# Performance work log

Measured on AMD Instinct MI355X. Metric: run time of the kernel, lower is better.

The kernel has to match this reference:

```python
import jax, jax.numpy as jnp
import numpy as np
import math

B, D, H, N, L = 32, 64, 8, 4096, 12
DK = D // H  # 8
APT = 10

def conv1x1_relu(x, w, b):
    # x: [B, C, N, L]; w: [O, C]; b: [O]  (1x1 conv == channel matmul)
    return jax.nn.relu(jnp.einsum('oc,bcnl->bonl', w, x) + b[None, :, None, None])

def setup_inputs() -> dict:
    key = jax.random.key(0)
    ks = jax.random.split(key, 12)
    s = 1.0 / math.sqrt(D)
    return {
        'x': jax.random.normal(ks[0], (B, D, N, L), jnp.float32),
        'wq': jax.random.normal(ks[1], (D, D), jnp.float32) * s,
        'bq': jnp.zeros((D,), jnp.float32),
        'wv': jax.random.normal(ks[2], (D, D), jnp.float32) * s,
        'bv': jnp.zeros((D,), jnp.float32),
        'wc': jax.random.normal(ks[3], (D, D), jnp.float32) * s,
        'bc': jnp.zeros((D,), jnp.float32),
        'memory': jax.random.normal(ks[4], (H, L, N, DK), jnp.float32) * 0.02,
        'weight': jnp.ones((D, N, L), jnp.float32),
        'bias': jnp.zeros((D, N, L), jnp.float32),
        'nv1': jax.random.normal(ks[5], (N, APT), jnp.float32),
        'nv2': jax.random.normal(ks[6], (APT, N), jnp.float32),
    }

def reference(x, wq, bq, wv, bv, wc, bc, memory, weight, bias, nv1, nv2):
    scale = 1.0 / math.sqrt(DK)
    q = conv1x1_relu(x, wq, bq)               # [B, D, N, L]
    v = conv1x1_relu(x, wv, bv)               # [B, D, N, L]
    # [B, D, N, L] -> [B, H, dk, N, L] -> [B, H, L, N, dk]
    v5 = jnp.transpose(v.reshape(B, H, DK, N, L), (0, 1, 4, 3, 2))
    q5 = jnp.transpose(q.reshape(B, H, DK, N, L), (0, 1, 4, 3, 2))
    key_sm = jax.nn.softmax(memory * scale, axis=-1)       # [H, L, N, dk]
    q_sm = jax.nn.softmax(q5 * scale, axis=-1)             # [B, H, L, N, dk]
    Aapt = jax.nn.softmax(jax.nn.relu(nv1 @ nv2), axis=-1) # [N, N]
    kv = jnp.einsum('hlnx,bhlny->bhlxy', key_sm, v5)       # [B,H,L,dk,dk]
    attn_qkv = jnp.einsum('bhlnx,bhlxy->bhlny', q_sm, kv)  # [B,H,L,N,dk]
    # 'nm,bhlnc->bhlnc' sums Aapt over m -> row-sum scaling of value
    row = jnp.sum(Aapt, axis=1)                            # [N]
    attn_dyn = row[None, None, None, :, None] * v5
    y = attn_qkv + attn_dyn                                # [B,H,L,N,dk]
    y = jnp.transpose(y, (0, 1, 4, 3, 2)).reshape(B, D, N, L)
    y = conv1x1_relu(y, wc, bc)
    out = y * weight[None] + bias[None] + y
    return out
```

## Files before the change

kernel.cpp:

```cpp
#include <hip/hip_runtime.h>
#include <math.h>

#define BB 32
#define DD 64
#define HH 8
#define NNN 4096
#define LL 12
#define PP (NNN * LL)

#define NTILES_A 24
#define CHUNK_A (64 * NTILES_A)
#define NCHUNK_A (PP / CHUNK_A)

#define NTILES_B 12
#define CHUNK_B (64 * NTILES_B)
#define NCHUNK_B (PP / CHUNK_B)

#define VSTRIDE 68
#define SCALE 0.35355339059327373f

__global__ void prep(const float* __restrict__ wq, const float* __restrict__ wv,
                     const float* __restrict__ wc, float* __restrict__ wt)
{
    const int i = blockIdx.x * 256 + threadIdx.x;
    const int o = i >> 6, c = i & 63;
    wt[c * 64 + o]        = wq[i];
    wt[4096 + c * 64 + o] = wv[i];
    wt[8192 + c * 64 + o] = wc[i];
}

__global__ void prep_ksm(const float* __restrict__ mem, float* __restrict__ ksm)
{
    const int g = blockIdx.x * 256 + threadIdx.x;
    const int p = g >> 3, h = g & 7;
    const int n = p / 12, l = p - n * 12;
    const float4* mp = (const float4*)(mem + (((size_t)(h * 12 + l) * NNN + n) << 3));
    float4 a0 = mp[0], a1 = mp[1];
    float v0 = a0.x * SCALE, v1 = a0.y * SCALE, v2 = a0.z * SCALE, v3 = a0.w * SCALE;
    float v4 = a1.x * SCALE, v5 = a1.y * SCALE, v6 = a1.z * SCALE, v7 = a1.w * SCALE;
    float m = fmaxf(fmaxf(fmaxf(v0, v1), fmaxf(v2, v3)),
                    fmaxf(fmaxf(v4, v5), fmaxf(v6, v7)));
    float e0 = __expf(v0 - m), e1 = __expf(v1 - m), e2 = __expf(v2 - m), e3 = __expf(v3 - m);
    float e4 = __expf(v4 - m), e5 = __expf(v5 - m), e6 = __expf(v6 - m), e7 = __expf(v7 - m);
    float inv = 1.0f / (e0 + e1 + e2 + e3 + e4 + e5 + e6 + e7);
    float4* op = (float4*)(ksm + ((size_t)g << 3));
    op[0] = make_float4(e0 * inv, e1 * inv, e2 * inv, e3 * inv);
    op[1] = make_float4(e4 * inv, e5 * inv, e6 * inv, e7 * inv);
}

__global__ __launch_bounds__(512, 8)
void pass_a(const float* __restrict__ x, const float* __restrict__ wvt,
            const float* __restrict__ bv, const float* __restrict__ mem,
            const float* __restrict__ ksm,
            float* __restrict__ kv)
{
    __shared__ float v_tile[64 * VSTRIDE];
    __shared__ float ks_tile[64 * VSTRIDE];

    const int t = threadIdx.x;
    const int b = blockIdx.y;
    const int chunk0 = blockIdx.x * CHUNK_A;

    const int p1 = t & 63;
    const int og = t >> 6;
    const int o0 = og << 3;
    const int o0u = __builtin_amdgcn_readfirstlane(o0);
    const float* __restrict__ wvu = wvt + o0u;

    float bvl[8];
#pragma unroll
    for (int j = 0; j < 8; j++) bvl[j] = bv[o0 + j];

    const int h2 = (t >> 3) & 7;
    const int x2 = t & 7;
    const int l0 = t >> 6;
    const int l1 = 8 + (t >> 6);
    const bool has2 = (t < 256);

    float acc[2][8];
#pragma unroll
    for (int q = 0; q < 2; q++)
#pragma unroll
        for (int y = 0; y < 8; y++) acc[q][y] = 0.f;

    const float* xb = x + (size_t)(b * 64) * PP;

    for (int tile = 0; tile < NTILES_A; tile++) {
        const int pbase = chunk0 + tile * 64;

        if (ksm) {
            const int pos = t >> 3, h = t & 7;
            const float4* kg = (const float4*)(ksm + (((size_t)(pbase + pos)) << 6) + (h << 3));
            float4 a0 = kg[0], a1 = kg[1];
            float4* kp = (float4*)(ks_tile + pos * VSTRIDE + (h << 3));
            kp[0] = a0; kp[1] = a1;
        } else {
            int pos = t >> 3, h = t & 7;
            int pg = pbase + pos;
            int n = pg / 12;
            int l = pg - n * 12;
            const float4* mp = (const float4*)(mem + (((size_t)(h * 12 + l) * NNN + n) << 3));
            float4 a0 = mp[0], a1 = mp[1];
            float v0 = a0.x * SCALE, v1 = a0.y * SCALE, v2 = a0.z * SCALE, v3 = a0.w * SCALE;
            float v4 = a1.x * SCALE, v5 = a1.y * SCALE, v6 = a1.z * SCALE, v7 = a1.w * SCALE;
            float m = fmaxf(fmaxf(fmaxf(v0, v1), fmaxf(v2, v3)),
                            fmaxf(fmaxf(v4, v5), fmaxf(v6, v7)));
            float e0 = __expf(v0 - m), e1 = __expf(v1 - m), e2 = __expf(v2 - m), e3 = __expf(v3 - m);
            float e4 = __expf(v4 - m), e5 = __expf(v5 - m), e6 = __expf(v6 - m), e7 = __expf(v7 - m);
            float inv = 1.0f / (e0 + e1 + e2 + e3 + e4 + e5 + e6 + e7);
            float4* kp = (float4*)(ks_tile + pos * VSTRIDE + (h << 3));
            kp[0] = make_float4(e0 * inv, e1 * inv, e2 * inv, e3 * inv);
            kp[1] = make_float4(e4 * inv, e5 * inv, e6 * inv, e7 * inv);
        }

        float va[8];
#pragma unroll
        for (int j = 0; j < 8; j++) va[j] = 0.f;
        const float* xp = xb + pbase + p1;
        for (int c = 0; c < 64; c += 4) {
            float xs0 = xp[(size_t)c * PP];
            float xs1 = xp[(size_t)(c + 1) * PP];
            float xs2 = xp[(size_t)(c + 2) * PP];
            float xs3 = xp[(size_t)(c + 3) * PP];
            const float* w0 = wvu + c * 64;
#pragma unroll
            for (int j = 0; j < 8; j++) {
                va[j] += w0[j] * xs0;
                va[j] += w0[64 + j] * xs1;
                va[j] += w0[128 + j] * xs2;
                va[j] += w0[192 + j] * xs3;
            }
        }
        float4* vt4 = (float4*)(v_tile + p1 * VSTRIDE + o0);
        {
            float4 w;
            w.x = fmaxf(va[0] + bvl[0], 0.f);
            w.y = fmaxf(va[1] + bvl[1], 0.f);
            w.z = fmaxf(va[2] + bvl[2], 0.f);
            w.w = fmaxf(va[3] + bvl[3], 0.f);
            vt4[0] = w;
            w.x = fmaxf(va[4] + bvl[4], 0.f);
            w.y = fmaxf(va[5] + bvl[5], 0.f);
            w.z = fmaxf(va[6] + bvl[6], 0.f);
            w.w = fmaxf(va[7] + bvl[7], 0.f);
            vt4[1] = w;
        }
        __syncthreads();

        const int r = pbase % 12;
        {
            int s = l0 - r;
            if (s < 0) s += 12;
            for (int p = s; p < 64; p += 12) {
                float ksv = ks_tile[p * VSTRIDE + (h2 << 3) + x2];
                const float4* vp = (const float4*)(v_tile + p * VSTRIDE + (h2 << 3));
                float4 u0 = vp[0], u1 = vp[1];
                acc[0][0] += ksv * u0.x; acc[0][1] += ksv * u0.y;
                acc[0][2] += ksv * u0.z; acc[0][3] += ksv * u0.w;
                acc[0][4] += ksv * u1.x; acc[0][5] += ksv * u1.y;
                acc[0][6] += ksv * u1.z; acc[0][7] += ksv * u1.w;
            }
        }
        if (has2) {
            int s = l1 - r;
            if (s < 0) s += 12;
            for (int p = s; p < 64; p += 12) {
                float ksv = ks_tile[p * VSTRIDE + (h2 << 3) + x2];
                const float4* vp = (const float4*)(v_tile + p * VSTRIDE + (h2 << 3));
                float4 u0 = vp[0], u1 = vp[1];
                acc[1][0] += ksv * u0.x; acc[1][1] += ksv * u0.y;
                acc[1][2] += ksv * u0.z; acc[1][3] += ksv * u0.w;
                acc[1][4] += ksv * u1.x; acc[1][5] += ksv * u1.y;
                acc[1][6] += ksv * u1.z; acc[1][7] += ksv * u1.w;
            }
        }
        __syncthreads();
    }

    {
        float* kvp = kv + (((size_t)((b * 12 + l0) * 8 + h2)) << 6) + (x2 << 3);
#pragma unroll
        for (int y = 0; y < 8; y++) atomicAdd(kvp + y, acc[0][y]);
    }
    if (has2) {
        float* kvp = kv + (((size_t)((b * 12 + l1) * 8 + h2)) << 6) + (x2 << 3);
#pragma unroll
        for (int y = 0; y < 8; y++) atomicAdd(kvp + y, acc[1][y]);
    }
}

__global__ __launch_bounds__(256, 4)
void pass_b(const float* __restrict__ x, const float* __restrict__ wqt,
            const float* __restrict__ wvt, const float* __restrict__ wct,
            const float* __restrict__ bq, const float* __restrict__ bv,
            const float* __restrict__ bc, const float* __restrict__ kv,
            const float* __restrict__ wgt, const float* __restrict__ bsa,
            float* __restrict__ out)
{
    __shared__ float y_tile[64 * VSTRIDE];

    const int t = threadIdx.x;
    const int b = blockIdx.y;
    const int chunk0 = blockIdx.x * CHUNK_B;

    const int p1 = t & 63;
    const int og = t >> 6;
    const int o0 = og << 4;
    const int o0u = __builtin_amdgcn_readfirstlane(o0);
    const float* __restrict__ wqu = wqt + o0u;
    const float* __restrict__ wvu = wvt + o0u;
    const float* __restrict__ wcu = wct + o0u;

    float bql[16], bvl[16], bcl[16];
#pragma unroll
    for (int j = 0; j < 16; j++) {
        bql[j] = bq[o0 + j];
        bvl[j] = bv[o0 + j];
        bcl[j] = bc[o0 + j];
    }

    const float* xb = x + (size_t)(b * 64) * PP;
    float* ob = out + (size_t)(b * 64) * PP;

    for (int tile = 0; tile < NTILES_B; tile++) {
        const int pbase = chunk0 + tile * 64;
        const int pg = pbase + p1;
        const int l = pg % 12;

        float qa[16], va[16];
#pragma unroll
        for (int j = 0; j < 16; j++) { qa[j] = 0.f; va[j] = 0.f; }
        const float* xp = xb + pg;
        for (int c = 0; c < 64; c += 4) {
            float xs0 = xp[(size_t)c * PP];
            float xs1 = xp[(size_t)(c + 1) * PP];
            float xs2 = xp[(size_t)(c + 2) * PP];
            float xs3 = xp[(size_t)(c + 3) * PP];
            const float* q0 = wqu + c * 64;
            const float* v0 = wvu + c * 64;
#pragma unroll
            for (int j = 0; j < 16; j++) {
                qa[j] += q0[j] * xs0;       va[j] += v0[j] * xs0;
                qa[j] += q0[64 + j] * xs1;  va[j] += v0[64 + j] * xs1;
                qa[j] += q0[128 + j] * xs2; va[j] += v0[128 + j] * xs2;
                qa[j] += q0[192 + j] * xs3; va[j] += v0[192 + j] * xs3;
            }
        }
#pragma unroll
        for (int j = 0; j < 16; j++) {
            qa[j] = fmaxf(qa[j] + bql[j], 0.f) * SCALE;
            va[j] = fmaxf(va[j] + bvl[j], 0.f);
        }

#pragma unroll
        for (int hh = 0; hh < 2; hh++) {
            float* qh = qa + hh * 8;
            float m = fmaxf(fmaxf(fmaxf(qh[0], qh[1]), fmaxf(qh[2], qh[3])),
                            fmaxf(fmaxf(qh[4], qh[5]), fmaxf(qh[6], qh[7])));
            float s = 0.f;
#pragma unroll
            for (int xk = 0; xk < 8; xk++) { qh[xk] = __expf(qh[xk] - m); s += qh[xk]; }
            float inv = 1.0f / s;
#pragma unroll
            for (int xk = 0; xk < 8; xk++) qh[xk] *= inv;
        }

#pragma unroll
        for (int hh = 0; hh < 2; hh++) {
            const int h = og * 2 + hh;
            const float* kvp = kv + (((size_t)((b * 12 + l) * 8 + h)) << 6);
            float yv[8];
#pragma unroll
            for (int y = 0; y < 8; y++) yv[y] = va[hh * 8 + y];
#pragma unroll
            for (int xk = 0; xk < 8; xk++) {
                float qv = qa[hh * 8 + xk];
                const float4* kp = (const float4*)(kvp + (xk << 3));
                float4 k0 = kp[0], k1 = kp[1];
                yv[0] += qv * k0.x; yv[1] += qv * k0.y;
                yv[2] += qv * k0.z; yv[3] += qv * k0.w;
                yv[4] += qv * k1.x; yv[5] += qv * k1.y;
                yv[6] += qv * k1.z; yv[7] += qv * k1.w;
            }
#pragma unroll
            for (int y = 0; y < 8; y++)
                y_tile[(o0 + hh * 8 + y) * VSTRIDE + p1] = yv[y];
        }
        __syncthreads();

        float ca[16];
#pragma unroll
        for (int j = 0; j < 16; j++) ca[j] = 0.f;
        for (int c = 0; c < 64; c += 4) {
            float y0 = y_tile[c * VSTRIDE + p1];
            float y1 = y_tile[(c + 1) * VSTRIDE + p1];
            float y2 = y_tile[(c + 2) * VSTRIDE + p1];
            float y3 = y_tile[(c + 3) * VSTRIDE + p1];
            const float* w0 = wcu + c * 64;
#pragma unroll
            for (int j = 0; j < 16; j++) {
                ca[j] += w0[j] * y0;
                ca[j] += w0[64 + j] * y1;
                ca[j] += w0[128 + j] * y2;
                ca[j] += w0[192 + j] * y3;
            }
        }
#pragma unroll
        for (int j = 0; j < 16; j++) {
            float yc = fmaxf(ca[j] + bcl[j], 0.f);
            size_t oi = (size_t)(o0 + j) * PP + pg;
            ob[oi] = yc * (wgt[oi] + 1.0f) + bsa[oi];
        }
        __syncthreads();
    }
}

extern "C" void kernel_launch(void* const* d_in, const int* in_sizes, int n_in,
                              void* d_out, int out_size, void* d_ws, size_t ws_size,
                              hipStream_t stream) {
    const float* x   = (const float*)d_in[0];
    const float* wq  = (const float*)d_in[1];
    const float* bq  = (const float*)d_in[2];
    const float* wv  = (const float*)d_in[3];
    const float* bv  = (const float*)d_in[4];
    const float* wc  = (const float*)d_in[5];
    const float* bc  = (const float*)d_in[6];
    const float* mem = (const float*)d_in[7];
    const float* wgt = (const float*)d_in[8];
    const float* bsa = (const float*)d_in[9];
    float* outp = (float*)d_out;

    const size_t kv_floats  = (size_t)BB * LL * HH * 64;
    const size_t wt_floats  = 3 * 4096;
    const size_t ksm_floats = (size_t)PP * 64;

    float* kvw = (float*)d_ws;
    float* wt  = kvw + kv_floats;
    float* ksm = wt + wt_floats;
    const bool have_ksm =
        ws_size >= (kv_floats + wt_floats + ksm_floats) * sizeof(float);

    hipMemsetAsync(kvw, 0, kv_floats * sizeof(float), stream);

    prep<<<16, 256, 0, stream>>>(wq, wv, wc, wt);
    if (have_ksm) {
        prep_ksm<<<(PP * 8) / 256, 256, 0, stream>>>(mem, ksm);
    }

    dim3 grid_a(NCHUNK_A, BB);
    pass_a<<<grid_a, 512, 0, stream>>>(x, wt + 4096, bv, mem,
                                       have_ksm ? ksm : nullptr, kvw);
    dim3 grid_b(NCHUNK_B, BB);
    pass_b<<<grid_b, 256, 0, stream>>>(x, wt, wt + 4096, wt + 8192,
                                       bq, bv, bc, kvw, wgt, bsa, outp);
}
```

Measured before the change: 1.915 ms.

## Stage x tiles through LDS with float4 loads in both passes

Both passes now load the 64x64 x tile cooperatively with vectorized float4 global loads into shared memory. Each thread then reads its channel values from LDS instead of doing strided scalar global loads, where several thread groups re-read the same x values. The existing LDS buffer is reused for both x and v/y, which costs extra barriers. pass_b's launch bound rises from 4 to 6 blocks per CU, so register spilling becomes a risk, and the ksm load pattern is remapped to match.

```diff
diff --git a/kernel.cpp b/kernel.cpp
--- a/kernel.cpp
+++ b/kernel.cpp
@@ -54,7 +54,7 @@
             const float* __restrict__ ksm,
             float* __restrict__ kv)
 {
-    __shared__ float v_tile[64 * VSTRIDE];
+    __shared__ float xv_tile[64 * VSTRIDE];
     __shared__ float ks_tile[64 * VSTRIDE];
 
     const int t = threadIdx.x;
@@ -71,6 +71,9 @@
 #pragma unroll
     for (int j = 0; j < 8; j++) bvl[j] = bv[o0 + j];
 
+    const int sx_c  = t >> 4;
+    const int sx_p4 = (t & 15) << 2;
+
     const int h2 = (t >> 3) & 7;
     const int x2 = t & 7;
     const int l0 = t >> 6;
@@ -89,11 +92,10 @@
         const int pbase = chunk0 + tile * 64;
 
         if (ksm) {
-            const int pos = t >> 3, h = t & 7;
-            const float4* kg = (const float4*)(ksm + (((size_t)(pbase + pos)) << 6) + (h << 3));
-            float4 a0 = kg[0], a1 = kg[1];
-            float4* kp = (float4*)(ks_tile + pos * VSTRIDE + (h << 3));
-            kp[0] = a0; kp[1] = a1;
+            const float4 k0 = *(const float4*)(ksm + (((size_t)(pbase + sx_c)) << 6) + sx_p4);
+            const float4 k1 = *(const float4*)(ksm + (((size_t)(pbase + 32 + sx_c)) << 6) + sx_p4);
+            *(float4*)(ks_tile + sx_c * VSTRIDE + sx_p4) = k0;
+            *(float4*)(ks_tile + (32 + sx_c) * VSTRIDE + sx_p4) = k1;
         } else {
             int pos = t >> 3, h = t & 7;
             int pg = pbase + pos;
@@ -113,15 +115,22 @@
             kp[1] = make_float4(e4 * inv, e5 * inv, e6 * inv, e7 * inv);
         }
 
+        {
+            const float4 a0 = *(const float4*)(xb + (size_t)sx_c * PP + pbase + sx_p4);
+            const float4 a1 = *(const float4*)(xb + (size_t)(sx_c + 32) * PP + pbase + sx_p4);
+            *(float4*)(xv_tile + sx_c * VSTRIDE + sx_p4) = a0;
+            *(float4*)(xv_tile + (sx_c + 32) * VSTRIDE + sx_p4) = a1;
+        }
+        __syncthreads();
+
         float va[8];
 #pragma unroll
         for (int j = 0; j < 8; j++) va[j] = 0.f;
-        const float* xp = xb + pbase + p1;
         for (int c = 0; c < 64; c += 4) {
-            float xs0 = xp[(size_t)c * PP];
-            float xs1 = xp[(size_t)(c + 1) * PP];
-            float xs2 = xp[(size_t)(c + 2) * PP];
-            float xs3 = xp[(size_t)(c + 3) * PP];
+            float xs0 = xv_tile[c * VSTRIDE + p1];
+            float xs1 = xv_tile[(c + 1) * VSTRIDE + p1];
+            float xs2 = xv_tile[(c + 2) * VSTRIDE + p1];
+            float xs3 = xv_tile[(c + 3) * VSTRIDE + p1];
             const float* w0 = wvu + c * 64;
 #pragma unroll
             for (int j = 0; j < 8; j++) {
@@ -131,8 +140,10 @@
                 va[j] += w0[192 + j] * xs3;
             }
         }
-        float4* vt4 = (float4*)(v_tile + p1 * VSTRIDE + o0);
+        __syncthreads();
+
         {
+            float4* vt4 = (float4*)(xv_tile + p1 * VSTRIDE + o0);
             float4 w;
             w.x = fmaxf(va[0] + bvl[0], 0.f);
             w.y = fmaxf(va[1] + bvl[1], 0.f);
@@ -153,7 +164,7 @@
             if (s < 0) s += 12;
             for (int p = s; p < 64; p += 12) {
                 float ksv = ks_tile[p * VSTRIDE + (h2 << 3) + x2];
-                const float4* vp = (const float4*)(v_tile + p * VSTRIDE + (h2 << 3));
+                const float4* vp = (const float4*)(xv_tile + p * VSTRIDE + (h2 << 3));
                 float4 u0 = vp[0], u1 = vp[1];
                 acc[0][0] += ksv * u0.x; acc[0][1] += ksv * u0.y;
                 acc[0][2] += ksv * u0.z; acc[0][3] += ksv * u0.w;
@@ -166,7 +177,7 @@
             if (s < 0) s += 12;
             for (int p = s; p < 64; p += 12) {
                 float ksv = ks_tile[p * VSTRIDE + (h2 << 3) + x2];
-                const float4* vp = (const float4*)(v_tile + p * VSTRIDE + (h2 << 3));
+                const float4* vp = (const float4*)(xv_tile + p * VSTRIDE + (h2 << 3));
                 float4 u0 = vp[0], u1 = vp[1];
                 acc[1][0] += ksv * u0.x; acc[1][1] += ksv * u0.y;
                 acc[1][2] += ksv * u0.z; acc[1][3] += ksv * u0.w;
@@ -189,7 +200,7 @@
     }
 }
 
-__global__ __launch_bounds__(256, 4)
+__global__ __launch_bounds__(256, 6)
 void pass_b(const float* __restrict__ x, const float* __restrict__ wqt,
             const float* __restrict__ wvt, const float* __restrict__ wct,
             const float* __restrict__ bq, const float* __restrict__ bv,
@@ -197,7 +208,7 @@
             const float* __restrict__ wgt, const float* __restrict__ bsa,
             float* __restrict__ out)
 {
-    __shared__ float y_tile[64 * VSTRIDE];
+    __shared__ float tile[64 * VSTRIDE];
 
     const int t = threadIdx.x;
     const int b = blockIdx.y;
@@ -211,6 +222,9 @@
     const float* __restrict__ wvu = wvt + o0u;
     const float* __restrict__ wcu = wct + o0u;
 
+    const int sx_c  = t >> 4;
+    const int sx_p4 = (t & 15) << 2;
+
     float bql[16], bvl[16], bcl[16];
 #pragma unroll
     for (int j = 0; j < 16; j++) {
@@ -222,20 +236,27 @@
     const float* xb = x + (size_t)(b * 64) * PP;
     float* ob = out + (size_t)(b * 64) * PP;
 
-    for (int tile = 0; tile < NTILES_B; tile++) {
-        const int pbase = chunk0 + tile * 64;
+    for (int tile_i = 0; tile_i < NTILES_B; tile_i++) {
+        const int pbase = chunk0 + tile_i * 64;
         const int pg = pbase + p1;
         const int l = pg % 12;
 
+#pragma unroll
+        for (int r = 0; r < 4; r++) {
+            const int c = r * 16 + sx_c;
+            const float4 a = *(const float4*)(xb + (size_t)c * PP + pbase + sx_p4);
+            *(float4*)(tile + c * VSTRIDE + sx_p4) = a;
+        }
+        __syncthreads();
+
         float qa[16], va[16];
 #pragma unroll
         for (int j = 0; j < 16; j++) { qa[j] = 0.f; va[j] = 0.f; }
-        const float* xp = xb + pg;
         for (int c = 0; c < 64; c += 4) {
-            float xs0 = xp[(size_t)c * PP];
-            float xs1 = xp[(size_t)(c + 1) * PP];
-            float xs2 = xp[(size_t)(c + 2) * PP];
-            float xs3 = xp[(size_t)(c + 3) * PP];
+            float xs0 = tile[c * VSTRIDE + p1];
+            float xs1 = tile[(c + 1) * VSTRIDE + p1];
+            float xs2 = tile[(c + 2) * VSTRIDE + p1];
+            float xs3 = tile[(c + 3) * VSTRIDE + p1];
             const float* q0 = wqu + c * 64;
             const float* v0 = wvu + c * 64;
 #pragma unroll
@@ -265,37 +286,41 @@
             for (int xk = 0; xk < 8; xk++) qh[xk] *= inv;
         }
 
+        float yv[2][8];
 #pragma unroll
         for (int hh = 0; hh < 2; hh++) {
             const int h = og * 2 + hh;
             const float* kvp = kv + (((size_t)((b * 12 + l) * 8 + h)) << 6);
-            float yv[8];
-#pragma unroll
-            for (int y = 0; y < 8; y++) yv[y] = va[hh * 8 + y];
+#pragma unroll
+            for (int y = 0; y < 8; y++) yv[hh][y] = va[hh * 8 + y];
 #pragma unroll
             for (int xk = 0; xk < 8; xk++) {
                 float qv = qa[hh * 8 + xk];
                 const float4* kp = (const float4*)(kvp + (xk << 3));
                 float4 k0 = kp[0], k1 = kp[1];
-                yv[0] += qv * k0.x; yv[1] += qv * k0.y;
-                yv[2] += qv * k0.z; yv[3] += qv * k0.w;
-                yv[4] += qv * k1.x; yv[5] += qv * k1.y;
-                yv[6] += qv * k1.z; yv[7] += qv * k1.w;
-            }
+                yv[hh][0] += qv * k0.x; yv[hh][1] += qv * k0.y;
+                yv[hh][2] += qv * k0.z; yv[hh][3] += qv * k0.w;
+                yv[hh][4] += qv * k1.x; yv[hh][5] += qv * k1.y;
+                yv[hh][6] += qv * k1.z; yv[hh][7] += qv * k1.w;
+            }
+        }
+        __syncthreads();
+
+#pragma unroll
+        for (int hh = 0; hh < 2; hh++)
 #pragma unroll
             for (int y = 0; y < 8; y++)
-                y_tile[(o0 + hh * 8 + y) * VSTRIDE + p1] = yv[y];
-        }
+                tile[(o0 + hh * 8 + y) * VSTRIDE + p1] = yv[hh][y];
         __syncthreads();
 
         float ca[16];
 #pragma unroll
         for (int j = 0; j < 16; j++) ca[j] = 0.f;
         for (int c = 0; c < 64; c += 4) {
-            float y0 = y_tile[c * VSTRIDE + p1];
-            float y1 = y_tile[(c + 1) * VSTRIDE + p1];
-            float y2 = y_tile[(c + 2) * VSTRIDE + p1];
-            float y3 = y_tile[(c + 3) * VSTRIDE + p1];
+            float y0 = tile[c * VSTRIDE + p1];
+            float y1 = tile[(c + 1) * VSTRIDE + p1];
+            float y2 = tile[(c + 2) * VSTRIDE + p1];
+            float y3 = tile[(c + 3) * VSTRIDE + p1];
             const float* w0 = wcu + c * 64;
 #pragma unroll
             for (int j = 0; j < 16; j++) {
```

After: 2.286 ms. +19.4%, slower.
